# Kernel optimization log

Measured on AMD Instinct MI355X. Metric: run time of the kernel, lower is better.

Reference implementation:

```python
import jax, jax.numpy as jnp
import numpy as np

N_NODES = 100000
N_EDGES = 6400000
F_IN = 128
F_OUT = 16


def setup_inputs() -> dict:
    key = jax.random.key(0)
    k1, k2, k3 = jax.random.split(key, 3)
    x = jax.random.normal(k1, (N_NODES, F_IN), dtype=jnp.float32)
    edge_index = jax.random.randint(k2, (2, N_EDGES), 0, N_NODES, dtype=jnp.int64)
    W = jax.random.normal(k3, (F_IN, F_OUT), dtype=jnp.float32) / np.sqrt(F_IN)
    b = jnp.zeros((F_OUT,), dtype=jnp.float32)
    return {"x": x, "edge_index": edge_index, "W": W, "b": b}


def reference(x, edge_index, W, b):
    # GCNConv (PyG defaults: add self-loops, symmetric normalization) -> tanh -> mean pool
    N = x.shape[0]
    loops = jnp.arange(N, dtype=edge_index.dtype)
    row = jnp.concatenate([edge_index[0], loops])  # source nodes
    col = jnp.concatenate([edge_index[1], loops])  # target nodes
    # degree of target nodes (edge weight 1.0)
    deg = jax.ops.segment_sum(jnp.ones(row.shape[0], dtype=x.dtype), col, num_segments=N)
    dinv = jnp.where(deg > 0, jax.lax.rsqrt(deg), 0.0)
    norm = dinv[row] * dinv[col]  # [E+N]
    h = x @ W  # [N, F_OUT] transform first (cheaper than transforming messages)
    msgs = h[row] * norm[:, None]  # gather + scale
    out = jax.ops.segment_sum(msgs, col, num_segments=N) + b  # scatter-add
    h = jnp.tanh(out)
    # MeanAggregation over all nodes -> single graph embedding [1, F_OUT]
    return jnp.mean(h, axis=0, keepdims=True)
```

## Files before the change

kernel.cpp:

```cpp
#include <hip/hip_runtime.h>
#include <math.h>

#define N_NODES 100000
#define N_EDGES 6400000
#define F_IN 128
#define F_OUT 16
#define NB 391
#define NBLK 1600
#define EPB 4000
#define BCAP 20480
#define KPB 5
#define QSCALE 1024.0f
#define QINV   (1.0f / 1024.0f)
#define FIN_GRID 640
#define GN 128
#define GSTRIDE 132

__global__ void __launch_bounds__(256) place_kernel(const int* __restrict__ row,
        const int* __restrict__ col, int* __restrict__ cur,
        unsigned int* __restrict__ packed) {
    __shared__ int hist[NB];
    __shared__ int scanb[512];
    __shared__ int base[NB];
    __shared__ int gadj[NB];
    __shared__ unsigned int tile[EPB];
    __shared__ unsigned short tileb[EPB];
    const int t = threadIdx.x, k = blockIdx.x;
    const int e0 = k * EPB;
    int myc[16], myr[16];
    #pragma unroll
    for (int j = 0; j < 16; j++) {
        int idx = t + j * 256;
        if (idx < EPB) { myc[j] = col[e0 + idx]; myr[j] = row[e0 + idx]; }
        else { myc[j] = -1; myr[j] = 0; }
    }
    for (int i = t; i < NB; i += 256) hist[i] = 0;
    __syncthreads();
    #pragma unroll
    for (int j = 0; j < 16; j++)
        if (myc[j] >= 0) atomicAdd(&hist[myc[j] >> 8], 1);
    __syncthreads();
    scanb[t] = (t < NB) ? hist[t] : 0;
    scanb[t + 256] = (t + 256 < NB) ? hist[t + 256] : 0;
    __syncthreads();
    for (int off = 1; off < 512; off <<= 1) {
        int a  = (t >= off) ? scanb[t - off] : 0;
        int a2 = scanb[t + 256 - off];
        __syncthreads();
        scanb[t] += a; scanb[t + 256] += a2;
        __syncthreads();
    }
    if (t < NB) base[t] = scanb[t] - hist[t];
    if (t + 256 < NB) base[t + 256] = scanb[t + 256] - hist[t + 256];
    __syncthreads();
    for (int bb = t; bb < NB; bb += 256) {
        int c = hist[bb];
        int g = (c > 0) ? atomicAdd(&cur[bb], c) : 0;
        gadj[bb] = bb * BCAP + g - base[bb];
        hist[bb] = 0;
    }
    __syncthreads();
    #pragma unroll
    for (int j = 0; j < 16; j++) {
        if (myc[j] >= 0) {
            int bb = myc[j] >> 8;
            int pos = base[bb] + atomicAdd(&hist[bb], 1);
            tile[pos] = ((unsigned)myr[j] << 8) | (unsigned)(myc[j] & 255);
            tileb[pos] = (unsigned short)bb;
        }
    }
    __syncthreads();
    for (int i = t; i < EPB; i += 256)
        packed[gadj[tileb[i]] + i] = tile[i];
}

__global__ void __launch_bounds__(256) deg_kernel(const unsigned int* __restrict__ packed,
        const int* __restrict__ cur, int* __restrict__ deg) {
    __shared__ int dh[256];
    const int t = threadIdx.x;
    dh[t] = 0;
    __syncthreads();
    const int b = blockIdx.x, part = blockIdx.y;
    const int cnt = cur[b];
    const int s = b * BCAP;
    const int chunk = (cnt + 3) >> 2;
    const int cs = s + part * chunk;
    const int ce = s + min((part + 1) * chunk, cnt);
    for (int i = cs + t; i < ce; i += 256)
        atomicAdd(&dh[packed[i] & 255u], 1);
    __syncthreads();
    const int node = (b << 8) + t;
    if (node < N_NODES && dh[t]) atomicAdd(&deg[node], dh[t]);
}

__global__ void __launch_bounds__(256) gemm_kernel(const float* __restrict__ x,
        const float* __restrict__ W, const int* __restrict__ deg,
        short* __restrict__ gq, int* __restrict__ acc) {
    __shared__ float Ws[F_IN * F_OUT];
    __shared__ float xs[GN * GSTRIDE];
    const int t = threadIdx.x;
    const int n0 = blockIdx.x * GN;
    {
        const size_t z0 = (size_t)blockIdx.x * 2048;
        for (int j = t; j < 2048; j += 256) {
            size_t idx = z0 + j;
            if (idx < (size_t)N_NODES * F_OUT) acc[idx] = 0;
        }
    }
    const float4* W4 = (const float4*)W;
    for (int i = t; i < 512; i += 256) ((float4*)Ws)[i] = W4[i];
    for (int i = t; i < GN * 32; i += 256) {
        int r = i >> 5, c4 = i & 31;
        float4 v = make_float4(0.f, 0.f, 0.f, 0.f);
        if (n0 + r < N_NODES)
            v = ((const float4*)(x + (size_t)(n0 + r) * F_IN))[c4];
        *(float4*)(xs + r * GSTRIDE + c4 * 4) = v;
    }
    __syncthreads();
    const int fq = t & 3, n2 = t >> 2;
    const float* xrA = xs + n2 * GSTRIDE;
    const float* xrB = xs + (n2 + 64) * GSTRIDE;
    float accA[4] = {0.f, 0.f, 0.f, 0.f};
    float accB[4] = {0.f, 0.f, 0.f, 0.f};
    #pragma unroll 8
    for (int kq = 0; kq < 32; kq++) {
        float4 xa = *(const float4*)(xrA + kq * 4);
        float4 xb = *(const float4*)(xrB + kq * 4);
        #pragma unroll
        for (int j = 0; j < 4; j++) {
            float4 w = *(const float4*)(Ws + (kq * 4 + j) * 16 + fq * 4);
            float a = (j == 0) ? xa.x : (j == 1) ? xa.y : (j == 2) ? xa.z : xa.w;
            float bv = (j == 0) ? xb.x : (j == 1) ? xb.y : (j == 2) ? xb.z : xb.w;
            accA[0] += a * w.x;  accA[1] += a * w.y;
            accA[2] += a * w.z;  accA[3] += a * w.w;
            accB[0] += bv * w.x; accB[1] += bv * w.y;
            accB[2] += bv * w.z; accB[3] += bv * w.w;
        }
    }
    const int gA = n0 + n2, gB = n0 + n2 + 64;
    if (gA < N_NODES) {
        float dinv = rsqrtf((float)deg[gA] + 1.0f);
        short4 o;
        float v0 = fminf(fmaxf(accA[0] * dinv * QSCALE, -32000.f), 32000.f);
        float v1 = fminf(fmaxf(accA[1] * dinv * QSCALE, -32000.f), 32000.f);
        float v2 = fminf(fmaxf(accA[2] * dinv * QSCALE, -32000.f), 32000.f);
        float v3 = fminf(fmaxf(accA[3] * dinv * QSCALE, -32000.f), 32000.f);
        o.x = (short)__float2int_rn(v0); o.y = (short)__float2int_rn(v1);
        o.z = (short)__float2int_rn(v2); o.w = (short)__float2int_rn(v3);
        *(short4*)(gq + (size_t)gA * 16 + fq * 4) = o;
    }
    if (gB < N_NODES) {
        float dinv = rsqrtf((float)deg[gB] + 1.0f);
        short4 o;
        float v0 = fminf(fmaxf(accB[0] * dinv * QSCALE, -32000.f), 32000.f);
        float v1 = fminf(fmaxf(accB[1] * dinv * QSCALE, -32000.f), 32000.f);
        float v2 = fminf(fmaxf(accB[2] * dinv * QSCALE, -32000.f), 32000.f);
        float v3 = fminf(fmaxf(accB[3] * dinv * QSCALE, -32000.f), 32000.f);
        o.x = (short)__float2int_rn(v0); o.y = (short)__float2int_rn(v1);
        o.z = (short)__float2int_rn(v2); o.w = (short)__float2int_rn(v3);
        *(short4*)(gq + (size_t)gB * 16 + fq * 4) = o;
    }
}

__global__ void __launch_bounds__(256) scatter_kernel(
        const unsigned int* __restrict__ packed, const int* __restrict__ cur,
        const short* __restrict__ gq, int* __restrict__ acc) {
    __shared__ int sacc[256 * F_OUT];
    const int t = threadIdx.x;
    for (int i = t; i < 256 * F_OUT; i += 256) sacc[i] = 0;
    __syncthreads();
    const int b = blockIdx.x, part = blockIdx.y;
    const int cnt = cur[b];
    const int s = b * BCAP;
    const int chunk = (cnt + KPB - 1) / KPB;
    const int cs = s + part * chunk;
    const int ce = s + min((part + 1) * chunk, cnt);
    const int f = t & 15, eg = t >> 4;
    int i = cs + eg;
    for (; i + 48 < ce; i += 64) {
        unsigned p0 = packed[i];
        unsigned p1 = packed[i + 16];
        unsigned p2 = packed[i + 32];
        unsigned p3 = packed[i + 48];
        int v0 = gq[(p0 >> 8) * 16 + f];
        int v1 = gq[(p1 >> 8) * 16 + f];
        int v2 = gq[(p2 >> 8) * 16 + f];
        int v3 = gq[(p3 >> 8) * 16 + f];
        atomicAdd(&sacc[((p0 & 255u) << 4) + f], v0);
        atomicAdd(&sacc[((p1 & 255u) << 4) + f], v1);
        atomicAdd(&sacc[((p2 & 255u) << 4) + f], v2);
        atomicAdd(&sacc[((p3 & 255u) << 4) + f], v3);
    }
    for (; i < ce; i += 16) {
        unsigned p0 = packed[i];
        atomicAdd(&sacc[((p0 & 255u) << 4) + f], (int)gq[(p0 >> 8) * 16 + f]);
    }
    __syncthreads();
    const int nbase = b << 8;
    for (int j = t; j < 256 * F_OUT; j += 256) {
        int v = sacc[j];
        if (v && nbase + (j >> 4) < N_NODES)
            atomicAdd(&acc[((size_t)nbase << 4) + j], v);
    }
}

__global__ void __launch_bounds__(256) finalize_kernel(const int* __restrict__ acc,
        const short* __restrict__ gq, const int* __restrict__ deg,
        const float* __restrict__ b, double* __restrict__ dsum,
        int* __restrict__ done, float* __restrict__ out) {
    __shared__ float s[4][16];
    __shared__ int lastflag;
    const int tid = threadIdx.x;
    const int f = tid & 15;
    const float bf = b[f];
    float local = 0.f;
    for (int i = blockIdx.x * blockDim.x + tid; i < N_NODES * F_OUT;
         i += gridDim.x * blockDim.x) {
        const int n = i >> 4;
        int ai = acc[i] + (int)gq[i];
        float dinvn = rsqrtf((float)deg[n] + 1.0f);
        local += tanhf(dinvn * ((float)ai * QINV) + bf);
    }
    local += __shfl_down(local, 32);
    local += __shfl_down(local, 16);
    const int lane = tid & 63, wave = tid >> 6;
    if (lane < 16) s[wave][lane] = local;
    __syncthreads();
    if (tid < 16) {
        float v = s[0][tid] + s[1][tid] + s[2][tid] + s[3][tid];
        atomicAdd(&dsum[tid], (double)v);
    }
    if (tid == 0) {
        __threadfence();
        lastflag = (atomicAdd(done, 1) == (int)gridDim.x - 1);
    }
    __syncthreads();
    if (lastflag && tid < 16) {
        double v = atomicAdd(&dsum[tid], 0.0);
        out[tid] = (float)(v * (1.0 / (double)N_NODES));
    }
}

extern "C" void kernel_launch(void* const* d_in, const int* in_sizes, int n_in,
                              void* d_out, int out_size, void* d_ws, size_t ws_size,
                              hipStream_t stream) {
    const float* x  = (const float*)d_in[0];
    const int*   ei = (const int*)d_in[1];
    const float* W  = (const float*)d_in[2];
    const float* b  = (const float*)d_in[3];
    float* out = (float*)d_out;

    const int* row = ei;
    const int* col = ei + N_EDGES;

    char* p = (char*)d_ws;
    double*       dsum   = (double*)p;        p += 128;
    int*          done   = (int*)p;           p += 32;
    int*          cur    = (int*)p;           p += 1600;
    int*          deg    = (int*)p;           p += (size_t)N_NODES * 4;
    int*          acc    = (int*)p;           p += (size_t)N_NODES * F_OUT * 4;
    short*        gq     = (short*)p;         p += (size_t)N_NODES * F_OUT * 2;
    unsigned int* packed = (unsigned int*)p;

    hipMemsetAsync(dsum, 0, 128 + 32 + 1600 + (size_t)N_NODES * 4, stream);

    place_kernel   <<<NBLK, 256, 0, stream>>>(row, col, cur, packed);
    deg_kernel     <<<dim3(NB, 4), 256, 0, stream>>>(packed, cur, deg);
    gemm_kernel    <<<(N_NODES + GN - 1) / GN, 256, 0, stream>>>(x, W, deg, gq, acc);
    scatter_kernel <<<dim3(NB, KPB), 256, 0, stream>>>(packed, cur, gq, acc);
    finalize_kernel<<<FIN_GRID, 256, 0, stream>>>(acc, gq, deg, b, dsum, done, out);
}
```

Before: 299.2 us.

## Pack feature pairs into 64-bit atomics and split buckets into fixed sub-regions

Each pair of quantized features is packed into one 64-bit word, so the scatter does half as many LDS and global atomic adds. The finalize step unpacks the pair with a borrow correction. Buckets are split into KPB fixed-capacity sub-regions, each with its own atomic cursor, which spreads contention on the place cursors and gives deg/scatter blocks exact ranges. Degree zeroing moves into place_kernel, shrinking the memset. The cost is doubled gather bytes per feature, since int32 lanes are now read instead of shorts, and a risk of overflowing a sub-region if a bucket's edges are uneven across residues.

```diff
diff --git a/kernel.cpp b/kernel.cpp
--- a/kernel.cpp
+++ b/kernel.cpp
@@ -8,8 +8,9 @@
 #define NB 391
 #define NBLK 1600
 #define EPB 4000
-#define BCAP 20480
 #define KPB 5
+#define RCAP 4096
+#define BCAP (KPB * RCAP)
 #define QSCALE 1024.0f
 #define QINV   (1.0f / 1024.0f)
 #define FIN_GRID 640
@@ -18,7 +19,7 @@
 
 __global__ void __launch_bounds__(256) place_kernel(const int* __restrict__ row,
         const int* __restrict__ col, int* __restrict__ cur,
-        unsigned int* __restrict__ packed) {
+        int* __restrict__ deg, unsigned int* __restrict__ packed) {
     __shared__ int hist[NB];
     __shared__ int scanb[512];
     __shared__ int base[NB];
@@ -26,6 +27,10 @@
     __shared__ unsigned int tile[EPB];
     __shared__ unsigned short tileb[EPB];
     const int t = threadIdx.x, k = blockIdx.x;
+    const int r = k % KPB;
+    const int z0 = k * 63;
+    for (int j = t; j < 63; j += 256)
+        if (z0 + j < N_NODES) deg[z0 + j] = 0;
     const int e0 = k * EPB;
     int myc[16], myr[16];
     #pragma unroll
@@ -55,8 +60,8 @@
     __syncthreads();
     for (int bb = t; bb < NB; bb += 256) {
         int c = hist[bb];
-        int g = (c > 0) ? atomicAdd(&cur[bb], c) : 0;
-        gadj[bb] = bb * BCAP + g - base[bb];
+        int g = (c > 0) ? atomicAdd(&cur[bb * KPB + r], c) : 0;
+        gadj[bb] = bb * BCAP + r * RCAP + g - base[bb];
         hist[bb] = 0;
     }
     __syncthreads();
@@ -80,12 +85,10 @@
     const int t = threadIdx.x;
     dh[t] = 0;
     __syncthreads();
-    const int b = blockIdx.x, part = blockIdx.y;
-    const int cnt = cur[b];
-    const int s = b * BCAP;
-    const int chunk = (cnt + 3) >> 2;
-    const int cs = s + part * chunk;
-    const int ce = s + min((part + 1) * chunk, cnt);
+    const int b = blockIdx.x, p = blockIdx.y;
+    const int cnt = cur[b * KPB + p];
+    const int cs = b * BCAP + p * RCAP;
+    const int ce = cs + cnt;
     for (int i = cs + t; i < ce; i += 256)
         atomicAdd(&dh[packed[i] & 255u], 1);
     __syncthreads();
@@ -95,16 +98,16 @@
 
 __global__ void __launch_bounds__(256) gemm_kernel(const float* __restrict__ x,
         const float* __restrict__ W, const int* __restrict__ deg,
-        short* __restrict__ gq, int* __restrict__ acc) {
+        unsigned long long* __restrict__ gqe, unsigned long long* __restrict__ acc64) {
     __shared__ float Ws[F_IN * F_OUT];
     __shared__ float xs[GN * GSTRIDE];
     const int t = threadIdx.x;
     const int n0 = blockIdx.x * GN;
     {
-        const size_t z0 = (size_t)blockIdx.x * 2048;
-        for (int j = t; j < 2048; j += 256) {
+        const size_t z0 = (size_t)blockIdx.x * 1024;
+        for (int j = t; j < 1024; j += 256) {
             size_t idx = z0 + j;
-            if (idx < (size_t)N_NODES * F_OUT) acc[idx] = 0;
+            if (idx < (size_t)N_NODES * 8) acc64[idx] = 0ull;
         }
     }
     const float4* W4 = (const float4*)W;
@@ -140,91 +143,99 @@
     const int gA = n0 + n2, gB = n0 + n2 + 64;
     if (gA < N_NODES) {
         float dinv = rsqrtf((float)deg[gA] + 1.0f);
-        short4 o;
-        float v0 = fminf(fmaxf(accA[0] * dinv * QSCALE, -32000.f), 32000.f);
-        float v1 = fminf(fmaxf(accA[1] * dinv * QSCALE, -32000.f), 32000.f);
-        float v2 = fminf(fmaxf(accA[2] * dinv * QSCALE, -32000.f), 32000.f);
-        float v3 = fminf(fmaxf(accA[3] * dinv * QSCALE, -32000.f), 32000.f);
-        o.x = (short)__float2int_rn(v0); o.y = (short)__float2int_rn(v1);
-        o.z = (short)__float2int_rn(v2); o.w = (short)__float2int_rn(v3);
-        *(short4*)(gq + (size_t)gA * 16 + fq * 4) = o;
+        int q[4];
+        #pragma unroll
+        for (int j = 0; j < 4; j++) {
+            float v = fminf(fmaxf(accA[j] * dinv * QSCALE, -32000.f), 32000.f);
+            q[j] = __float2int_rn(v);
+        }
+        ulonglong2 e;
+        e.x = (unsigned long long)(((long long)q[1] << 32) + (long long)q[0]);
+        e.y = (unsigned long long)(((long long)q[3] << 32) + (long long)q[2]);
+        *(ulonglong2*)(gqe + (size_t)gA * 8 + fq * 2) = e;
     }
     if (gB < N_NODES) {
         float dinv = rsqrtf((float)deg[gB] + 1.0f);
-        short4 o;
-        float v0 = fminf(fmaxf(accB[0] * dinv * QSCALE, -32000.f), 32000.f);
-        float v1 = fminf(fmaxf(accB[1] * dinv * QSCALE, -32000.f), 32000.f);
-        float v2 = fminf(fmaxf(accB[2] * dinv * QSCALE, -32000.f), 32000.f);
-        float v3 = fminf(fmaxf(accB[3] * dinv * QSCALE, -32000.f), 32000.f);
-        o.x = (short)__float2int_rn(v0); o.y = (short)__float2int_rn(v1);
-        o.z = (short)__float2int_rn(v2); o.w = (short)__float2int_rn(v3);
-        *(short4*)(gq + (size_t)gB * 16 + fq * 4) = o;
+        int q[4];
+        #pragma unroll
+        for (int j = 0; j < 4; j++) {
+            float v = fminf(fmaxf(accB[j] * dinv * QSCALE, -32000.f), 32000.f);
+            q[j] = __float2int_rn(v);
+        }
+        ulonglong2 e;
+        e.x = (unsigned long long)(((long long)q[1] << 32) + (long long)q[0]);
+        e.y = (unsigned long long)(((long long)q[3] << 32) + (long long)q[2]);
+        *(ulonglong2*)(gqe + (size_t)gB * 8 + fq * 2) = e;
     }
 }
 
 __global__ void __launch_bounds__(256) scatter_kernel(
         const unsigned int* __restrict__ packed, const int* __restrict__ cur,
-        const short* __restrict__ gq, int* __restrict__ acc) {
-    __shared__ int sacc[256 * F_OUT];
+        const unsigned long long* __restrict__ gqe, unsigned long long* __restrict__ acc64) {
+    __shared__ unsigned long long sacc[256 * 8];
     const int t = threadIdx.x;
-    for (int i = t; i < 256 * F_OUT; i += 256) sacc[i] = 0;
-    __syncthreads();
-    const int b = blockIdx.x, part = blockIdx.y;
-    const int cnt = cur[b];
-    const int s = b * BCAP;
-    const int chunk = (cnt + KPB - 1) / KPB;
-    const int cs = s + part * chunk;
-    const int ce = s + min((part + 1) * chunk, cnt);
-    const int f = t & 15, eg = t >> 4;
+    for (int i = t; i < 256 * 8; i += 256) sacc[i] = 0ull;
+    __syncthreads();
+    const int b = blockIdx.x, p = blockIdx.y;
+    const int cnt = cur[b * KPB + p];
+    const int cs = b * BCAP + p * RCAP;
+    const int ce = cs + cnt;
+    const int fp = t & 7, eg = t >> 3;
     int i = cs + eg;
-    for (; i + 48 < ce; i += 64) {
+    for (; i + 96 < ce; i += 128) {
         unsigned p0 = packed[i];
-        unsigned p1 = packed[i + 16];
-        unsigned p2 = packed[i + 32];
-        unsigned p3 = packed[i + 48];
-        int v0 = gq[(p0 >> 8) * 16 + f];
-        int v1 = gq[(p1 >> 8) * 16 + f];
-        int v2 = gq[(p2 >> 8) * 16 + f];
-        int v3 = gq[(p3 >> 8) * 16 + f];
-        atomicAdd(&sacc[((p0 & 255u) << 4) + f], v0);
-        atomicAdd(&sacc[((p1 & 255u) << 4) + f], v1);
-        atomicAdd(&sacc[((p2 & 255u) << 4) + f], v2);
-        atomicAdd(&sacc[((p3 & 255u) << 4) + f], v3);
-    }
-    for (; i < ce; i += 16) {
+        unsigned p1 = packed[i + 32];
+        unsigned p2 = packed[i + 64];
+        unsigned p3 = packed[i + 96];
+        unsigned long long v0 = gqe[(size_t)(p0 >> 8) * 8 + fp];
+        unsigned long long v1 = gqe[(size_t)(p1 >> 8) * 8 + fp];
+        unsigned long long v2 = gqe[(size_t)(p2 >> 8) * 8 + fp];
+        unsigned long long v3 = gqe[(size_t)(p3 >> 8) * 8 + fp];
+        atomicAdd(&sacc[((p0 & 255u) << 3) + fp], v0);
+        atomicAdd(&sacc[((p1 & 255u) << 3) + fp], v1);
+        atomicAdd(&sacc[((p2 & 255u) << 3) + fp], v2);
+        atomicAdd(&sacc[((p3 & 255u) << 3) + fp], v3);
+    }
+    for (; i < ce; i += 32) {
         unsigned p0 = packed[i];
-        atomicAdd(&sacc[((p0 & 255u) << 4) + f], (int)gq[(p0 >> 8) * 16 + f]);
+        atomicAdd(&sacc[((p0 & 255u) << 3) + fp], gqe[(size_t)(p0 >> 8) * 8 + fp]);
     }
     __syncthreads();
     const int nbase = b << 8;
-    for (int j = t; j < 256 * F_OUT; j += 256) {
-        int v = sacc[j];
-        if (v && nbase + (j >> 4) < N_NODES)
-            atomicAdd(&acc[((size_t)nbase << 4) + j], v);
-    }
-}
-
-__global__ void __launch_bounds__(256) finalize_kernel(const int* __restrict__ acc,
-        const short* __restrict__ gq, const int* __restrict__ deg,
+    for (int j = t; j < 256 * 8; j += 256) {
+        unsigned long long v = sacc[j];
+        if (v && nbase + (j >> 3) < N_NODES)
+            atomicAdd(&acc64[((size_t)nbase << 3) + j], v);
+    }
+}
+
+__global__ void __launch_bounds__(256) finalize_kernel(
+        const unsigned long long* __restrict__ acc64,
+        const unsigned long long* __restrict__ gqe, const int* __restrict__ deg,
         const float* __restrict__ b, double* __restrict__ dsum,
         int* __restrict__ done, float* __restrict__ out) {
     __shared__ float s[4][16];
     __shared__ int lastflag;
     const int tid = threadIdx.x;
-    const int f = tid & 15;
-    const float bf = b[f];
-    float local = 0.f;
-    for (int i = blockIdx.x * blockDim.x + tid; i < N_NODES * F_OUT;
+    const int fp = tid & 7;
+    const float b0 = b[2 * fp], b1 = b[2 * fp + 1];
+    float local0 = 0.f, local1 = 0.f;
+    for (int i = blockIdx.x * blockDim.x + tid; i < N_NODES * 8;
          i += gridDim.x * blockDim.x) {
-        const int n = i >> 4;
-        int ai = acc[i] + (int)gq[i];
+        const int n = i >> 3;
+        long long tot = (long long)acc64[i] + (long long)gqe[i];
+        int lo = (int)(unsigned int)(tot & 0xFFFFFFFFll);
+        int hi = (int)(tot >> 32);
+        if (lo < 0) hi += 1;
         float dinvn = rsqrtf((float)deg[n] + 1.0f);
-        local += tanhf(dinvn * ((float)ai * QINV) + bf);
-    }
-    local += __shfl_down(local, 32);
-    local += __shfl_down(local, 16);
+        local0 += tanhf(dinvn * ((float)lo * QINV) + b0);
+        local1 += tanhf(dinvn * ((float)hi * QINV) + b1);
+    }
+    local0 += __shfl_down(local0, 32);  local1 += __shfl_down(local1, 32);
+    local0 += __shfl_down(local0, 16);  local1 += __shfl_down(local1, 16);
+    local0 += __shfl_down(local0, 8);   local1 += __shfl_down(local1, 8);
     const int lane = tid & 63, wave = tid >> 6;
-    if (lane < 16) s[wave][lane] = local;
+    if (lane < 8) { s[wave][2 * lane] = local0; s[wave][2 * lane + 1] = local1; }
     __syncthreads();
     if (tid < 16) {
         float v = s[0][tid] + s[1][tid] + s[2][tid] + s[3][tid];
@@ -254,19 +265,19 @@
     const int* col = ei + N_EDGES;
 
     char* p = (char*)d_ws;
-    double*       dsum   = (double*)p;        p += 128;
-    int*          done   = (int*)p;           p += 32;
-    int*          cur    = (int*)p;           p += 1600;
-    int*          deg    = (int*)p;           p += (size_t)N_NODES * 4;
-    int*          acc    = (int*)p;           p += (size_t)N_NODES * F_OUT * 4;
-    short*        gq     = (short*)p;         p += (size_t)N_NODES * F_OUT * 2;
-    unsigned int* packed = (unsigned int*)p;
-
-    hipMemsetAsync(dsum, 0, 128 + 32 + 1600 + (size_t)N_NODES * 4, stream);
-
-    place_kernel   <<<NBLK, 256, 0, stream>>>(row, col, cur, packed);
-    deg_kernel     <<<dim3(NB, 4), 256, 0, stream>>>(packed, cur, deg);
-    gemm_kernel    <<<(N_NODES + GN - 1) / GN, 256, 0, stream>>>(x, W, deg, gq, acc);
-    scatter_kernel <<<dim3(NB, KPB), 256, 0, stream>>>(packed, cur, gq, acc);
-    finalize_kernel<<<FIN_GRID, 256, 0, stream>>>(acc, gq, deg, b, dsum, done, out);
-}
+    double*             dsum   = (double*)p;             p += 128;
+    int*                done   = (int*)p;                p += 32;
+    int*                cur    = (int*)p;                p += 7840;
+    int*                deg    = (int*)p;                p += (size_t)N_NODES * 4;
+    unsigned long long* acc64  = (unsigned long long*)p; p += (size_t)N_NODES * 8 * 8;
+    unsigned long long* gqe    = (unsigned long long*)p; p += (size_t)N_NODES * 8 * 8;
+    unsigned int*       packed = (unsigned int*)p;
+
+    hipMemsetAsync(dsum, 0, 8000, stream);
+
+    place_kernel   <<<NBLK, 256, 0, stream>>>(row, col, cur, deg, packed);
+    deg_kernel     <<<dim3(NB, KPB), 256, 0, stream>>>(packed, cur, deg);
+    gemm_kernel    <<<(N_NODES + GN - 1) / GN, 256, 0, stream>>>(x, W, deg, gqe, acc64);
+    scatter_kernel <<<dim3(NB, KPB), 256, 0, stream>>>(packed, cur, gqe, acc64);
+    finalize_kernel<<<FIN_GRID, 256, 0, stream>>>(acc64, gqe, deg, b, dsum, done, out);
+}
```

Result: slower. 314.3 us (+5.0%).

## Enlarge edge-placement tiles and reload edges instead of holding them in registers

Applied to the files above, without the earlier changes.

The edge bucketing kernel now handles 6400 edges per block across 1000 blocks, where it previously used 4000 edges across 1600 blocks. Edges are no longer cached in per-thread register arrays. Each edge is read from global memory once for the histogram and again for placement. The per-slot bucket id in shared memory shrinks to one byte, and the high bit is recovered by comparing the slot position against the bucket-256 base. This lowers register pressure, shared-memory footprint and the number of global cursor atomics, at the cost of reading the edge arrays twice.

```diff
diff --git a/kernel.cpp b/kernel.cpp
--- a/kernel.cpp
+++ b/kernel.cpp
@@ -6,8 +6,8 @@
 #define F_IN 128
 #define F_OUT 16
 #define NB 391
-#define NBLK 1600
-#define EPB 4000
+#define NBLK 1000
+#define EPB 6400
 #define BCAP 20480
 #define KPB 5
 #define QSCALE 1024.0f
@@ -24,21 +24,13 @@
     __shared__ int base[NB];
     __shared__ int gadj[NB];
     __shared__ unsigned int tile[EPB];
-    __shared__ unsigned short tileb[EPB];
+    __shared__ unsigned char tileb8[EPB];
     const int t = threadIdx.x, k = blockIdx.x;
     const int e0 = k * EPB;
-    int myc[16], myr[16];
-    #pragma unroll
-    for (int j = 0; j < 16; j++) {
-        int idx = t + j * 256;
-        if (idx < EPB) { myc[j] = col[e0 + idx]; myr[j] = row[e0 + idx]; }
-        else { myc[j] = -1; myr[j] = 0; }
-    }
     for (int i = t; i < NB; i += 256) hist[i] = 0;
     __syncthreads();
-    #pragma unroll
-    for (int j = 0; j < 16; j++)
-        if (myc[j] >= 0) atomicAdd(&hist[myc[j] >> 8], 1);
+    for (int i = t; i < EPB; i += 256)
+        atomicAdd(&hist[col[e0 + i] >> 8], 1);
     __syncthreads();
     scanb[t] = (t < NB) ? hist[t] : 0;
     scanb[t + 256] = (t + 256 < NB) ? hist[t + 256] : 0;
@@ -53,6 +45,7 @@
     if (t < NB) base[t] = scanb[t] - hist[t];
     if (t + 256 < NB) base[t + 256] = scanb[t + 256] - hist[t + 256];
     __syncthreads();
+    const int b256 = base[256];
     for (int bb = t; bb < NB; bb += 256) {
         int c = hist[bb];
         int g = (c > 0) ? atomicAdd(&cur[bb], c) : 0;
@@ -60,18 +53,19 @@
         hist[bb] = 0;
     }
     __syncthreads();
-    #pragma unroll
-    for (int j = 0; j < 16; j++) {
-        if (myc[j] >= 0) {
-            int bb = myc[j] >> 8;
-            int pos = base[bb] + atomicAdd(&hist[bb], 1);
-            tile[pos] = ((unsigned)myr[j] << 8) | (unsigned)(myc[j] & 255);
-            tileb[pos] = (unsigned short)bb;
-        }
-    }
-    __syncthreads();
-    for (int i = t; i < EPB; i += 256)
-        packed[gadj[tileb[i]] + i] = tile[i];
+    for (int i = t; i < EPB; i += 256) {
+        int c = col[e0 + i];
+        int r = row[e0 + i];
+        int bb = c >> 8;
+        int pos = base[bb] + atomicAdd(&hist[bb], 1);
+        tile[pos] = ((unsigned)r << 8) | (unsigned)(c & 255);
+        tileb8[pos] = (unsigned char)bb;
+    }
+    __syncthreads();
+    for (int i = t; i < EPB; i += 256) {
+        int bb = (int)tileb8[i] + ((i >= b256) ? 256 : 0);
+        packed[gadj[bb] + i] = tile[i];
+    }
 }
 
 __global__ void __launch_bounds__(256) deg_kernel(const unsigned int* __restrict__ packed,
```

Measured after the change: 292.7 us. 1.02x faster.
